# Kernel tuning notes

Hardware: AMD Instinct MI355X
Metric: run time of the kernel (lower is better)

The kernel has to match this reference:

```python
import jax, jax.numpy as jnp
import numpy as np

NUM_HEADS = 16
BLOCK_SIZE = 64


def setup_inputs() -> dict:
    key = jax.random.key(0)
    ks = jax.random.split(key, 5)
    B, S, C = 2, 2047, 1024
    return {
        "x": jax.random.normal(ks[0], (B, S, C), dtype=jnp.float32),
        "global_token": jax.random.normal(ks[1], (1, 1, C), dtype=jnp.float32),
        "qkv_w": jax.random.normal(ks[2], (3 * C, C), dtype=jnp.float32) * 0.02,
        "proj_w": jax.random.normal(ks[3], (C, C), dtype=jnp.float32) * 0.02,
        "proj_b": jax.random.normal(ks[4], (C,), dtype=jnp.float32) * 0.02,
    }


def reference(x, global_token, qkv_w, proj_w, proj_b):
    B, S, C = x.shape
    H = NUM_HEADS
    D = C // H
    scale = D ** -0.5
    # prepend global token -> N = S + 1
    g = jnp.broadcast_to(global_token, (B, 1, C))
    xg = jnp.concatenate([g, x], axis=1)
    N = S + 1
    # fused qkv projection (torch Linear: x @ W^T)
    qkv = (xg @ qkv_w.T).reshape(B, N, 3, H, D)
    qkv = jnp.transpose(qkv, (2, 0, 3, 1, 4))  # [3, B, H, N, D]
    q, k, v = qkv[0], qkv[1], qkv[2]
    # block-causal mask: query t sees key j iff block(j) <= block(t)
    blk = jnp.arange(N) // BLOCK_SIZE
    mask = blk[:, None] >= blk[None, :]  # [N, N]
    attn = jnp.einsum("bhqd,bhkd->bhqk", q, k) * scale
    attn = jnp.where(mask[None, None], attn, -jnp.inf)
    attn = jax.nn.softmax(attn, axis=-1)
    out = jnp.einsum("bhqk,bhkd->bhqd", attn, v)
    out = jnp.transpose(out, (0, 2, 1, 3)).reshape(B, N, C)
    out = out[:, 1:, :]  # drop global token
    return out @ proj_w.T + proj_b
```

## Files before the change

kernel.cpp:

```cpp
#include <hip/hip_runtime.h>
#include <math.h>

typedef _Float16 h16;
typedef _Float16 half8 __attribute__((ext_vector_type(8)));
typedef float f32x4 __attribute__((ext_vector_type(4)));

#define NB 2
#define NS 2047
#define NC 1024
#define NN 2048
#define NH 16
#define ND 64

__device__ __forceinline__ void gl_lds16(const h16* g, h16* l) {
  __builtin_amdgcn_global_load_lds((const __attribute__((address_space(1))) void*)g,
                                   (__attribute__((address_space(3))) void*)l, 16, 0, 0);
}
__device__ __forceinline__ f32x4 mfma16(half8 a, half8 b, f32x4 c) {
  return __builtin_amdgcn_mfma_f32_16x16x32_f16(a, b, c, 0, 0, 0);
}

__global__ __launch_bounds__(256) void cast_xg_k(
    const float* __restrict__ x, const float* __restrict__ g, h16* __restrict__ out) {
  size_t i = ((size_t)blockIdx.x * 256 + threadIdx.x) * 16;
  const int c = (int)(i & (NC - 1));
  const int n = (int)((i >> 10) & (NN - 1));
  const int b = (int)(i >> 21);
  const float* src = (n == 0) ? (g + c) : (x + ((size_t)b * NS + (n - 1)) * NC + c);
  h16 tmp[16];
#pragma unroll
  for (int j = 0; j < 4; ++j) {
    float4 f = ((const float4*)src)[j];
    tmp[4 * j + 0] = (h16)f.x; tmp[4 * j + 1] = (h16)f.y;
    tmp[4 * j + 2] = (h16)f.z; tmp[4 * j + 3] = (h16)f.w;
  }
  *(half8*)(out + i) = *(half8*)&tmp[0];
  *(half8*)(out + i + 8) = *(half8*)&tmp[8];
}

__global__ __launch_bounds__(256) void cast_f16_k(
    const float* __restrict__ in, h16* __restrict__ out) {
  size_t i = ((size_t)blockIdx.x * 256 + threadIdx.x) * 8;
  float4 f0 = ((const float4*)(in + i))[0];
  float4 f1 = ((const float4*)(in + i))[1];
  h16 tmp[8];
  tmp[0] = (h16)f0.x; tmp[1] = (h16)f0.y; tmp[2] = (h16)f0.z; tmp[3] = (h16)f0.w;
  tmp[4] = (h16)f1.x; tmp[5] = (h16)f1.y; tmp[6] = (h16)f1.z; tmp[7] = (h16)f1.w;
  *(half8*)(out + i) = *(half8*)&tmp[0];
}

__global__ __launch_bounds__(256) void gemm_qkv_h(
    const h16* __restrict__ A, const h16* __restrict__ W, h16* __restrict__ out) {
  __shared__ h16 As[128 * 32];
  __shared__ h16 Bs[128 * 32];
  const int tid = threadIdx.x;
  const int m0 = blockIdx.y * 128, j0 = blockIdx.x * 128;
  const int wid = tid >> 6, lane = tid & 63, l15 = lane & 15, quad = lane >> 4;
  const h16* ag = A + (size_t)(m0 + wid * 32 + (lane >> 2)) * NC + (lane & 3) * 8;
  const h16* bg = W + (size_t)(j0 + wid * 32 + (lane >> 2)) * NC + (lane & 3) * 8;
  h16* lA = &As[wid * 32 * 32];
  h16* lB = &Bs[wid * 32 * 32];
  f32x4 acc[2][8];
#pragma unroll
  for (int rt = 0; rt < 2; ++rt)
#pragma unroll
    for (int ct = 0; ct < 8; ++ct) acc[rt][ct] = (f32x4){0.f, 0.f, 0.f, 0.f};

  for (int k0 = 0; k0 < NC; k0 += 32) {
    __syncthreads();
    gl_lds16(ag + k0, lA);
    gl_lds16(ag + k0 + 16 * NC, lA + 16 * 32);
    gl_lds16(bg + k0, lB);
    gl_lds16(bg + k0 + 16 * NC, lB + 16 * 32);
    __syncthreads();
    half8 af0 = *(const half8*)&As[(wid * 32 + l15) * 32 + quad * 8];
    half8 af1 = *(const half8*)&As[(wid * 32 + 16 + l15) * 32 + quad * 8];
#pragma unroll
    for (int ct = 0; ct < 8; ++ct) {
      half8 bf = *(const half8*)&Bs[(ct * 16 + l15) * 32 + quad * 8];
      acc[0][ct] = mfma16(af0, bf, acc[0][ct]);
      acc[1][ct] = mfma16(af1, bf, acc[1][ct]);
    }
  }
#pragma unroll
  for (int rt = 0; rt < 2; ++rt)
#pragma unroll
    for (int ct = 0; ct < 8; ++ct)
#pragma unroll
      for (int r = 0; r < 4; ++r) {
        const int mm = m0 + wid * 32 + rt * 16 + quad * 4 + r;
        const int jj = j0 + ct * 16 + l15;
        out[(size_t)mm * (3 * NC) + jj] = (h16)acc[rt][ct][r];
      }
}

__global__ __launch_bounds__(256) void vtrans_k(
    const h16* __restrict__ qkvh, h16* __restrict__ vT) {
  __shared__ h16 ts[64 * 72];
  const int kb = blockIdx.x, h = blockIdx.y, b = blockIdx.z;
  const int t = threadIdx.x;
  const int key = t >> 2, co = (t & 3) * 16;
  const h16* src = qkvh + (size_t)(b * NN + kb * 64 + key) * (3 * NC) + 2 * NC + h * ND + co;
  half8 v0 = *(const half8*)src;
  half8 v1 = *(const half8*)(src + 8);
  *(half8*)&ts[key * 72 + co] = v0;
  *(half8*)&ts[key * 72 + co + 8] = v1;
  __syncthreads();
  const int d = t >> 2, ko = (t & 3) * 16;
  h16 buf[16];
#pragma unroll
  for (int i = 0; i < 16; ++i) buf[i] = ts[(ko + i) * 72 + d];
  h16* dst = vT + ((size_t)(b * NH + h) * ND + d) * NN + kb * 64 + ko;
  *(half8*)dst = *(half8*)&buf[0];
  *(half8*)(dst + 8) = *(half8*)&buf[8];
}

__device__ __forceinline__ void attn_tile(
    half8 aq0, half8 aq1, const h16* Ks, const h16* Vs, h16* Pw,
    int l15, int quad, f32x4* o, float* den) {
  f32x4 s[4];
#pragma unroll
  for (int ct = 0; ct < 4; ++ct) {
    half8 bk0 = *(const half8*)&Ks[(ct * 16 + l15) * 72 + quad * 8];
    half8 bk1 = *(const half8*)&Ks[(ct * 16 + l15) * 72 + 32 + quad * 8];
    f32x4 z = (f32x4){0.f, 0.f, 0.f, 0.f};
    z = mfma16(aq0, bk0, z);
    s[ct] = mfma16(aq1, bk1, z);
  }
#pragma unroll
  for (int ct = 0; ct < 4; ++ct)
#pragma unroll
    for (int r = 0; r < 4; ++r) {
      float p = __expf(s[ct][r] * 0.125f);
      den[r] += p;
      Pw[(quad * 4 + r) * 72 + ct * 16 + l15] = (h16)p;
    }
  half8 ap0 = *(const half8*)&Pw[l15 * 72 + quad * 8];
  half8 ap1 = *(const half8*)&Pw[l15 * 72 + 32 + quad * 8];
#pragma unroll
  for (int ct = 0; ct < 4; ++ct) {
    half8 bv0 = *(const half8*)&Vs[(ct * 16 + l15) * 72 + quad * 8];
    half8 bv1 = *(const half8*)&Vs[(ct * 16 + l15) * 72 + 32 + quad * 8];
    o[ct] = mfma16(ap0, bv0, o[ct]);
    o[ct] = mfma16(ap1, bv1, o[ct]);
  }
}

__global__ __launch_bounds__(256) void attn_h(
    const h16* __restrict__ qkvh, const h16* __restrict__ vT, h16* __restrict__ outp) {
  __shared__ h16 Ks[64 * 72];
  __shared__ h16 Vs[64 * 72];
  __shared__ h16 Ps[128 * 72];
  const int q1 = blockIdx.x;
  const int q2 = 31 - q1;
  const int h = blockIdx.y, b = blockIdx.z;
  const int tid = threadIdx.x, wid = tid >> 6, lane = tid & 63;
  const int l15 = lane & 15, quad = lane >> 4;
  const h16* q1src = qkvh + (size_t)(b * NN + q1 * 64 + wid * 16 + l15) * (3 * NC) + h * ND + quad * 8;
  const h16* q2src = qkvh + (size_t)(b * NN + q2 * 64 + wid * 16 + l15) * (3 * NC) + h * ND + quad * 8;
  half8 a1q0 = *(const half8*)q1src;
  half8 a1q1 = *(const half8*)(q1src + 32);
  half8 a2q0 = *(const half8*)q2src;
  half8 a2q1 = *(const half8*)(q2src + 32);
  f32x4 o1[4], o2[4];
  float d1[4] = {0.f, 0.f, 0.f, 0.f}, d2[4] = {0.f, 0.f, 0.f, 0.f};
#pragma unroll
  for (int ct = 0; ct < 4; ++ct) {
    o1[ct] = (f32x4){0.f, 0.f, 0.f, 0.f};
    o2[ct] = (f32x4){0.f, 0.f, 0.f, 0.f};
  }
  const int skey = tid >> 2, sco = (tid & 3) * 16;
  const h16* kbase = qkvh + (size_t)(b * NN + skey) * (3 * NC) + NC + h * ND + sco;
  const h16* vbase = vT + ((size_t)(b * NH + h) * ND + skey) * NN + sco;
  h16* P1 = &Ps[(wid * 16) * 72];
  h16* P2 = &Ps[(64 + wid * 16) * 72];

  for (int kb = 0; kb <= q2; ++kb) {
    const h16* kp = kbase + (size_t)kb * 64 * (3 * NC);
    half8 k0 = *(const half8*)kp;
    half8 k1 = *(const half8*)(kp + 8);
    const h16* vp = vbase + kb * 64;
    half8 v0 = *(const half8*)vp;
    half8 v1 = *(const half8*)(vp + 8);
    __syncthreads();
    *(half8*)&Ks[skey * 72 + sco] = k0; *(half8*)&Ks[skey * 72 + sco + 8] = k1;
    *(half8*)&Vs[skey * 72 + sco] = v0; *(half8*)&Vs[skey * 72 + sco + 8] = v1;
    __syncthreads();
    attn_tile(a2q0, a2q1, Ks, Vs, P2, l15, quad, o2, d2);
    if (kb <= q1) attn_tile(a1q0, a1q1, Ks, Vs, P1, l15, quad, o1, d1);
  }
#pragma unroll
  for (int r = 0; r < 4; ++r)
#pragma unroll
    for (int off = 1; off < 16; off <<= 1) {
      d1[r] += __shfl_xor(d1[r], off);
      d2[r] += __shfl_xor(d2[r], off);
    }
#pragma unroll
  for (int ct = 0; ct < 4; ++ct)
#pragma unroll
    for (int r = 0; r < 4; ++r) {
      const int n1 = q1 * 64 + wid * 16 + quad * 4 + r;
      const int n2 = q2 * 64 + wid * 16 + quad * 4 + r;
      outp[(size_t)(b * NN + n1) * NC + h * ND + ct * 16 + l15] = (h16)(o1[ct][r] / d1[r]);
      outp[(size_t)(b * NN + n2) * NC + h * ND + ct * 16 + l15] = (h16)(o2[ct][r] / d2[r]);
    }
}

__global__ __launch_bounds__(256) void gemm_proj_h(
    const h16* __restrict__ Ah, const h16* __restrict__ W,
    const float* __restrict__ bias, float* __restrict__ out) {
  __shared__ h16 As[64 * 32];
  __shared__ h16 Bs[128 * 32];
  const int tid = threadIdx.x;
  const int m0 = blockIdx.y * 64, j0 = blockIdx.x * 128;
  const int wid = tid >> 6, lane = tid & 63, l15 = lane & 15, quad = lane >> 4;
  int m = m0 + wid * 16 + (lane >> 2);
  if (m > NB * NS - 1) m = NB * NS - 1;
  const int bb = (m >= NS) ? 1 : 0;
  const h16* ag = Ah + (size_t)(bb * NN + m - bb * NS + 1) * NC + (lane & 3) * 8;
  const h16* bg = W + (size_t)(j0 + wid * 32 + (lane >> 2)) * NC + (lane & 3) * 8;
  h16* lA = &As[wid * 16 * 32];
  h16* lB = &Bs[wid * 32 * 32];
  f32x4 acc[8];
#pragma unroll
  for (int ct = 0; ct < 8; ++ct) acc[ct] = (f32x4){0.f, 0.f, 0.f, 0.f};

  for (int k0 = 0; k0 < NC; k0 += 32) {
    __syncthreads();
    gl_lds16(ag + k0, lA);
    gl_lds16(bg + k0, lB);
    gl_lds16(bg + k0 + 16 * NC, lB + 16 * 32);
    __syncthreads();
    half8 af = *(const half8*)&As[(wid * 16 + l15) * 32 + quad * 8];
#pragma unroll
    for (int ct = 0; ct < 8; ++ct) {
      half8 bf = *(const half8*)&Bs[(ct * 16 + l15) * 32 + quad * 8];
      acc[ct] = mfma16(af, bf, acc[ct]);
    }
  }
#pragma unroll
  for (int ct = 0; ct < 8; ++ct) {
    const float bv = bias[j0 + ct * 16 + l15];
#pragma unroll
    for (int r = 0; r < 4; ++r) {
      const int mm = m0 + wid * 16 + quad * 4 + r;
      if (mm < NB * NS)
        out[(size_t)mm * NC + j0 + ct * 16 + l15] = acc[ct][r] + bv;
    }
  }
}

extern "C" void kernel_launch(void* const* d_in, const int* in_sizes, int n_in,
                              void* d_out, int out_size, void* d_ws, size_t ws_size,
                              hipStream_t stream) {
  const float* x = (const float*)d_in[0];
  const float* g = (const float*)d_in[1];
  const float* qkv_w = (const float*)d_in[2];
  const float* proj_w = (const float*)d_in[3];
  const float* proj_b = (const float*)d_in[4];
  float* out = (float*)d_out;

  h16* xgh  = (h16*)d_ws;
  h16* w3h  = xgh + (size_t)NB * NN * NC;
  h16* wph  = w3h + (size_t)3 * NC * NC;
  h16* qkvh = wph + (size_t)NC * NC;
  h16* vTh  = qkvh + (size_t)NB * NN * 3 * NC;
  h16* attnh = vTh + (size_t)NB * NH * ND * NN;

  cast_xg_k<<<dim3(1024), 256, 0, stream>>>(x, g, xgh);
  cast_f16_k<<<dim3(1536), 256, 0, stream>>>(qkv_w, w3h);
  cast_f16_k<<<dim3(512), 256, 0, stream>>>(proj_w, wph);
  gemm_qkv_h<<<dim3(24, 32), 256, 0, stream>>>(xgh, w3h, qkvh);
  vtrans_k<<<dim3(32, NH, NB), 256, 0, stream>>>(qkvh, vTh);
  attn_h<<<dim3(16, NH, NB), 256, 0, stream>>>(qkvh, vTh, attnh);
  gemm_proj_h<<<dim3(8, 64), 256, 0, stream>>>(attnh, wph, proj_b, out);
}
```

Measured before the change: 204.0 us.

## Split attention KV loop across two blocks with merge kernel, prefetch K/V, fuse weight casts

The attention kernel now splits each query-pair's key-block loop between two blocks by even/odd key block. Each block writes unnormalized partial outputs and row denominators, and a new merge kernel sums and normalizes them. This doubles the attention grid to fill more CUs (512 blocks instead of 256), and the next K/V tile is prefetched into registers while the current tile is computed. A shared P buffer and a launch-bounds occupancy hint shrink LDS use. The two weight-cast launches are also fused into one, at the cost of an extra merge pass and more intermediate memory traffic.

```diff
diff --git a/kernel.cpp b/kernel.cpp
--- a/kernel.cpp
+++ b/kernel.cpp
@@ -38,11 +38,12 @@
   *(half8*)(out + i + 8) = *(half8*)&tmp[8];
 }
 
-__global__ __launch_bounds__(256) void cast_f16_k(
-    const float* __restrict__ in, h16* __restrict__ out) {
+__global__ __launch_bounds__(256) void cast_w_k(
+    const float* __restrict__ qw, const float* __restrict__ pw, h16* __restrict__ out) {
   size_t i = ((size_t)blockIdx.x * 256 + threadIdx.x) * 8;
-  float4 f0 = ((const float4*)(in + i))[0];
-  float4 f1 = ((const float4*)(in + i))[1];
+  const float* src = (i < (size_t)3 * NC * NC) ? (qw + i) : (pw + (i - (size_t)3 * NC * NC));
+  float4 f0 = ((const float4*)src)[0];
+  float4 f1 = ((const float4*)src)[1];
   h16 tmp[8];
   tmp[0] = (h16)f0.x; tmp[1] = (h16)f0.y; tmp[2] = (h16)f0.z; tmp[3] = (h16)f0.w;
   tmp[4] = (h16)f1.x; tmp[5] = (h16)f1.y; tmp[6] = (h16)f1.z; tmp[7] = (h16)f1.w;
@@ -146,13 +147,15 @@
   }
 }
 
-__global__ __launch_bounds__(256) void attn_h(
-    const h16* __restrict__ qkvh, const h16* __restrict__ vT, h16* __restrict__ outp) {
+__global__ __launch_bounds__(256, 4) void attn_h(
+    const h16* __restrict__ qkvh, const h16* __restrict__ vT,
+    h16* __restrict__ Op0, h16* __restrict__ Op1, float* __restrict__ denp) {
   __shared__ h16 Ks[64 * 72];
   __shared__ h16 Vs[64 * 72];
-  __shared__ h16 Ps[128 * 72];
-  const int q1 = blockIdx.x;
-  const int q2 = 31 - q1;
+  __shared__ h16 Ps[64 * 72];
+  const int pr = blockIdx.x & 15;
+  const int c = blockIdx.x >> 4;
+  const int q1 = pr, q2 = 31 - pr;
   const int h = blockIdx.y, b = blockIdx.z;
   const int tid = threadIdx.x, wid = tid >> 6, lane = tid & 63;
   const int l15 = lane & 15, quad = lane >> 4;
@@ -172,22 +175,26 @@
   const int skey = tid >> 2, sco = (tid & 3) * 16;
   const h16* kbase = qkvh + (size_t)(b * NN + skey) * (3 * NC) + NC + h * ND + sco;
   const h16* vbase = vT + ((size_t)(b * NH + h) * ND + skey) * NN + sco;
-  h16* P1 = &Ps[(wid * 16) * 72];
-  h16* P2 = &Ps[(64 + wid * 16) * 72];
-
-  for (int kb = 0; kb <= q2; ++kb) {
-    const h16* kp = kbase + (size_t)kb * 64 * (3 * NC);
-    half8 k0 = *(const half8*)kp;
-    half8 k1 = *(const half8*)(kp + 8);
-    const h16* vp = vbase + kb * 64;
-    half8 v0 = *(const half8*)vp;
-    half8 v1 = *(const half8*)(vp + 8);
+  h16* Pw = &Ps[(wid * 16) * 72];
+
+  int kb = c;
+  const h16* kp = kbase + (size_t)kb * (64 * 3 * NC);
+  const h16* vp = vbase + kb * 64;
+  half8 k0 = *(const half8*)kp, k1 = *(const half8*)(kp + 8);
+  half8 v0 = *(const half8*)vp, v1 = *(const half8*)(vp + 8);
+
+  for (; kb <= q2; kb += 2) {
     __syncthreads();
     *(half8*)&Ks[skey * 72 + sco] = k0; *(half8*)&Ks[skey * 72 + sco + 8] = k1;
     *(half8*)&Vs[skey * 72 + sco] = v0; *(half8*)&Vs[skey * 72 + sco + 8] = v1;
     __syncthreads();
-    attn_tile(a2q0, a2q1, Ks, Vs, P2, l15, quad, o2, d2);
-    if (kb <= q1) attn_tile(a1q0, a1q1, Ks, Vs, P1, l15, quad, o1, d1);
+    const int nkb = (kb + 2 <= q2) ? (kb + 2) : kb;
+    kp = kbase + (size_t)nkb * (64 * 3 * NC);
+    vp = vbase + nkb * 64;
+    k0 = *(const half8*)kp; k1 = *(const half8*)(kp + 8);
+    v0 = *(const half8*)vp; v1 = *(const half8*)(vp + 8);
+    attn_tile(a2q0, a2q1, Ks, Vs, Pw, l15, quad, o2, d2);
+    if (kb <= q1) attn_tile(a1q0, a1q1, Ks, Vs, Pw, l15, quad, o1, d1);
   }
 #pragma unroll
   for (int r = 0; r < 4; ++r)
@@ -196,15 +203,40 @@
       d1[r] += __shfl_xor(d1[r], off);
       d2[r] += __shfl_xor(d2[r], off);
     }
+  h16* op = (c == 0) ? Op0 : Op1;
+  const size_t rbase = (size_t)(b * NH + h) * NN;
+  float* dch = denp + (size_t)c * (NB * NH * NN);
 #pragma unroll
   for (int ct = 0; ct < 4; ++ct)
 #pragma unroll
     for (int r = 0; r < 4; ++r) {
       const int n1 = q1 * 64 + wid * 16 + quad * 4 + r;
       const int n2 = q2 * 64 + wid * 16 + quad * 4 + r;
-      outp[(size_t)(b * NN + n1) * NC + h * ND + ct * 16 + l15] = (h16)(o1[ct][r] / d1[r]);
-      outp[(size_t)(b * NN + n2) * NC + h * ND + ct * 16 + l15] = (h16)(o2[ct][r] / d2[r]);
-    }
+      op[(rbase + n1) * ND + ct * 16 + l15] = (h16)o1[ct][r];
+      op[(rbase + n2) * ND + ct * 16 + l15] = (h16)o2[ct][r];
+      if (ct == 0 && l15 == 0) {
+        dch[rbase + n1] = d1[r];
+        dch[rbase + n2] = d2[r];
+      }
+    }
+}
+
+__global__ __launch_bounds__(256) void merge_k(
+    const h16* __restrict__ Op0, const h16* __restrict__ Op1,
+    const float* __restrict__ denp, h16* __restrict__ attnh) {
+  const size_t t = (size_t)blockIdx.x * 256 + threadIdx.x;
+  const int d = (int)(t & 7) * 8;
+  const size_t row = t >> 3;
+  half8 a = *(const half8*)(Op0 + row * ND + d);
+  half8 bb8 = *(const half8*)(Op1 + row * ND + d);
+  const float inv = 1.f / (denp[row] + denp[(size_t)NB * NH * NN + row]);
+  h16 o[8];
+#pragma unroll
+  for (int j = 0; j < 8; ++j) o[j] = (h16)(((float)a[j] + (float)bb8[j]) * inv);
+  const int n = (int)(row & (NN - 1));
+  const int h = (int)((row >> 11) & (NH - 1));
+  const int b = (int)(row >> 15);
+  *(half8*)(attnh + (size_t)(b * NN + n) * NC + h * ND + d) = *(half8*)&o[0];
 }
 
 __global__ __launch_bounds__(256) void gemm_proj_h(
@@ -267,12 +299,15 @@
   h16* qkvh = wph + (size_t)NC * NC;
   h16* vTh  = qkvh + (size_t)NB * NN * 3 * NC;
   h16* attnh = vTh + (size_t)NB * NH * ND * NN;
+  h16* op1  = attnh + (size_t)NB * NN * NC;
+  float* den = (float*)(op1 + (size_t)NB * NN * NC);
+  h16* op0 = xgh;
 
   cast_xg_k<<<dim3(1024), 256, 0, stream>>>(x, g, xgh);
-  cast_f16_k<<<dim3(1536), 256, 0, stream>>>(qkv_w, w3h);
-  cast_f16_k<<<dim3(512), 256, 0, stream>>>(proj_w, wph);
+  cast_w_k<<<dim3(2048), 256, 0, stream>>>(qkv_w, proj_w, w3h);
   gemm_qkv_h<<<dim3(24, 32), 256, 0, stream>>>(xgh, w3h, qkvh);
   vtrans_k<<<dim3(32, NH, NB), 256, 0, stream>>>(qkvh, vTh);
-  attn_h<<<dim3(16, NH, NB), 256, 0, stream>>>(qkvh, vTh, attnh);
+  attn_h<<<dim3(32, NH, NB), 256, 0, stream>>>(qkvh, vTh, op0, op1, den);
+  merge_k<<<dim3(2048), 256, 0, stream>>>(op0, op1, den, attnh);
   gemm_proj_h<<<dim3(8, 64), 256, 0, stream>>>(attnh, wph, proj_b, out);
 }
```

After: 251.9 us. 23.5% more time.

## Double-buffer attention K/V via direct LDS loads and keep P in registers

Applied to the files above, without the earlier changes.

Rewrites the attention kernel to prefetch the next K/V tile with global_load_lds into a swizzled double buffer, so loads overlap compute and each iteration needs one barrier instead of two. It computes S transposed (K as the A operand) and redistributes the packed fp16 probabilities through lane shuffles rather than an LDS round-trip, and folds the softmax scale into Q. The output is staged through LDS so each row is written with 16-byte stores. It also merges the two weight cast kernels into one launch and flattens the attention grid with a launch bound of 2 blocks per SM.

```diff
diff --git a/kernel.cpp b/kernel.cpp
--- a/kernel.cpp
+++ b/kernel.cpp
@@ -3,6 +3,7 @@
 
 typedef _Float16 h16;
 typedef _Float16 half8 __attribute__((ext_vector_type(8)));
+typedef _Float16 half2t __attribute__((ext_vector_type(2)));
 typedef float f32x4 __attribute__((ext_vector_type(4)));
 
 #define NB 2
@@ -38,11 +39,12 @@
   *(half8*)(out + i + 8) = *(half8*)&tmp[8];
 }
 
-__global__ __launch_bounds__(256) void cast_f16_k(
-    const float* __restrict__ in, h16* __restrict__ out) {
+__global__ __launch_bounds__(256) void cast_w_k(
+    const float* __restrict__ qw, const float* __restrict__ pw, h16* __restrict__ out) {
   size_t i = ((size_t)blockIdx.x * 256 + threadIdx.x) * 8;
-  float4 f0 = ((const float4*)(in + i))[0];
-  float4 f1 = ((const float4*)(in + i))[1];
+  const float* src = (i < (size_t)3 * NC * NC) ? (qw + i) : (pw + (i - (size_t)3 * NC * NC));
+  float4 f0 = ((const float4*)src)[0];
+  float4 f1 = ((const float4*)src)[1];
   h16 tmp[8];
   tmp[0] = (h16)f0.x; tmp[1] = (h16)f0.y; tmp[2] = (h16)f0.z; tmp[3] = (h16)f0.w;
   tmp[4] = (h16)f1.x; tmp[5] = (h16)f1.y; tmp[6] = (h16)f1.z; tmp[7] = (h16)f1.w;
@@ -115,96 +117,139 @@
   *(half8*)(dst + 8) = *(half8*)&buf[8];
 }
 
-__device__ __forceinline__ void attn_tile(
-    half8 aq0, half8 aq1, const h16* Ks, const h16* Vs, h16* Pw,
-    int l15, int quad, f32x4* o, float* den) {
-  f32x4 s[4];
+__global__ __launch_bounds__(256, 2) void attn_h(
+    const h16* __restrict__ qkvh, const h16* __restrict__ vT, h16* __restrict__ outp) {
+  __shared__ h16 KV[4][64 * 64];
+  const int wg = blockIdx.x;
+  const int pr = wg >> 5;
+  const int bh = wg & 31;
+  const int b = bh >> 4, h = bh & 15;
+  const int q1 = pr, q2 = 31 - pr;
+  const int tid = threadIdx.x, w = tid >> 6, lane = tid & 63;
+  const int l15 = lane & 15, quad = lane >> 4;
+
+  const int srow = w * 8 + (lane >> 3);
+  const int schunk = (lane & 7) ^ (srow & 7);
+  const h16* kq = qkvh + ((size_t)(b * NN + srow) * 3 + 1) * NC + h * ND + schunk * 8;
+  const h16* vq = vT + ((size_t)(b * NH + h) * ND + srow) * NN + schunk * 8;
+  const int ldso = w * 512;
+
+  const h16* q1src = qkvh + (size_t)(b * NN + q1 * 64 + w * 16 + l15) * (3 * NC) + h * ND + quad * 8;
+  const h16* q2src = qkvh + (size_t)(b * NN + q2 * 64 + w * 16 + l15) * (3 * NC) + h * ND + quad * 8;
+  half8 b1lo = *(const half8*)q1src, b1hi = *(const half8*)(q1src + 32);
+  half8 b2lo = *(const half8*)q2src, b2hi = *(const half8*)(q2src + 32);
+  b1lo *= (h16)0.125f; b1hi *= (h16)0.125f;
+  b2lo *= (h16)0.125f; b2hi *= (h16)0.125f;
+
+  int aoff[4][2];
 #pragma unroll
   for (int ct = 0; ct < 4; ++ct) {
-    half8 bk0 = *(const half8*)&Ks[(ct * 16 + l15) * 72 + quad * 8];
-    half8 bk1 = *(const half8*)&Ks[(ct * 16 + l15) * 72 + 32 + quad * 8];
-    f32x4 z = (f32x4){0.f, 0.f, 0.f, 0.f};
-    z = mfma16(aq0, bk0, z);
-    s[ct] = mfma16(aq1, bk1, z);
-  }
-#pragma unroll
-  for (int ct = 0; ct < 4; ++ct)
-#pragma unroll
-    for (int r = 0; r < 4; ++r) {
-      float p = __expf(s[ct][r] * 0.125f);
-      den[r] += p;
-      Pw[(quad * 4 + r) * 72 + ct * 16 + l15] = (h16)p;
-    }
-  half8 ap0 = *(const half8*)&Pw[l15 * 72 + quad * 8];
-  half8 ap1 = *(const half8*)&Pw[l15 * 72 + 32 + quad * 8];
-#pragma unroll
-  for (int ct = 0; ct < 4; ++ct) {
-    half8 bv0 = *(const half8*)&Vs[(ct * 16 + l15) * 72 + quad * 8];
-    half8 bv1 = *(const half8*)&Vs[(ct * 16 + l15) * 72 + 32 + quad * 8];
-    o[ct] = mfma16(ap0, bv0, o[ct]);
-    o[ct] = mfma16(ap1, bv1, o[ct]);
-  }
-}
-
-__global__ __launch_bounds__(256) void attn_h(
-    const h16* __restrict__ qkvh, const h16* __restrict__ vT, h16* __restrict__ outp) {
-  __shared__ h16 Ks[64 * 72];
-  __shared__ h16 Vs[64 * 72];
-  __shared__ h16 Ps[128 * 72];
-  const int q1 = blockIdx.x;
-  const int q2 = 31 - q1;
-  const int h = blockIdx.y, b = blockIdx.z;
-  const int tid = threadIdx.x, wid = tid >> 6, lane = tid & 63;
-  const int l15 = lane & 15, quad = lane >> 4;
-  const h16* q1src = qkvh + (size_t)(b * NN + q1 * 64 + wid * 16 + l15) * (3 * NC) + h * ND + quad * 8;
-  const h16* q2src = qkvh + (size_t)(b * NN + q2 * 64 + wid * 16 + l15) * (3 * NC) + h * ND + quad * 8;
-  half8 a1q0 = *(const half8*)q1src;
-  half8 a1q1 = *(const half8*)(q1src + 32);
-  half8 a2q0 = *(const half8*)q2src;
-  half8 a2q1 = *(const half8*)(q2src + 32);
+    const int r = ct * 16 + l15;
+    aoff[ct][0] = r * 64 + ((quad ^ (l15 & 7)) * 8);
+    aoff[ct][1] = r * 64 + (((quad + 4) ^ (l15 & 7)) * 8);
+  }
+  const int L0 = ((quad & 1) << 5) + l15;
+  const int L1 = L0 + 16;
+  const bool cs = ((quad >> 1) & 1) != 0;
+
   f32x4 o1[4], o2[4];
-  float d1[4] = {0.f, 0.f, 0.f, 0.f}, d2[4] = {0.f, 0.f, 0.f, 0.f};
+  float den1 = 0.f, den2 = 0.f;
 #pragma unroll
   for (int ct = 0; ct < 4; ++ct) {
     o1[ct] = (f32x4){0.f, 0.f, 0.f, 0.f};
     o2[ct] = (f32x4){0.f, 0.f, 0.f, 0.f};
   }
-  const int skey = tid >> 2, sco = (tid & 3) * 16;
-  const h16* kbase = qkvh + (size_t)(b * NN + skey) * (3 * NC) + NC + h * ND + sco;
-  const h16* vbase = vT + ((size_t)(b * NH + h) * ND + skey) * NN + sco;
-  h16* P1 = &Ps[(wid * 16) * 72];
-  h16* P2 = &Ps[(64 + wid * 16) * 72];
-
+
+  h16 *Kc = &KV[0][0], *Vc = &KV[1][0], *Kn = &KV[2][0], *Vn = &KV[3][0];
+
+#define STAGE(Kd, Vd, kb)                                              \
+  {                                                                    \
+    const h16* kp_ = kq + (size_t)(kb) * (64 * 3 * NC);                \
+    const h16* vp_ = vq + (kb)*64;                                     \
+    gl_lds16(kp_, (Kd) + ldso);                                        \
+    gl_lds16(kp_ + (size_t)32 * 3 * NC, (Kd) + 2048 + ldso);           \
+    gl_lds16(vp_, (Vd) + ldso);                                        \
+    gl_lds16(vp_ + 32 * NN, (Vd) + 2048 + ldso);                       \
+  }
+
+#define TILE(bqlo, bqhi, o, den)                                        \
+  {                                                                     \
+    f32x4 s_[4];                                                        \
+    _Pragma("unroll") for (int ct = 0; ct < 4; ++ct) {                  \
+      f32x4 z_ = (f32x4){0.f, 0.f, 0.f, 0.f};                           \
+      z_ = mfma16(kA[ct][0], bqlo, z_);                                 \
+      s_[ct] = mfma16(kA[ct][1], bqhi, z_);                             \
+    }                                                                   \
+    int pk_[4][2];                                                      \
+    _Pragma("unroll") for (int ct = 0; ct < 4; ++ct) {                  \
+      float e0 = __expf(s_[ct][0]), e1 = __expf(s_[ct][1]);             \
+      float e2 = __expf(s_[ct][2]), e3 = __expf(s_[ct][3]);             \
+      den += (e0 + e1) + (e2 + e3);                                     \
+      pk_[ct][0] = __builtin_bit_cast(int, __builtin_amdgcn_cvt_pkrtz(e0, e1)); \
+      pk_[ct][1] = __builtin_bit_cast(int, __builtin_amdgcn_cvt_pkrtz(e2, e3)); \
+    }                                                                   \
+    int a0 = __shfl(pk_[0][0], L0), a1 = __shfl(pk_[0][1], L0);         \
+    int a2 = __shfl(pk_[0][0], L1), a3 = __shfl(pk_[0][1], L1);         \
+    int c0 = __shfl(pk_[1][0], L0), c1 = __shfl(pk_[1][1], L0);         \
+    int c2 = __shfl(pk_[1][0], L1), c3 = __shfl(pk_[1][1], L1);         \
+    int4 f0i = make_int4(cs ? c0 : a0, cs ? c1 : a1, cs ? c2 : a2, cs ? c3 : a3); \
+    a0 = __shfl(pk_[2][0], L0); a1 = __shfl(pk_[2][1], L0);             \
+    a2 = __shfl(pk_[2][0], L1); a3 = __shfl(pk_[2][1], L1);             \
+    c0 = __shfl(pk_[3][0], L0); c1 = __shfl(pk_[3][1], L0);             \
+    c2 = __shfl(pk_[3][0], L1); c3 = __shfl(pk_[3][1], L1);             \
+    int4 f1i = make_int4(cs ? c0 : a0, cs ? c1 : a1, cs ? c2 : a2, cs ? c3 : a3); \
+    half8 pf0 = __builtin_bit_cast(half8, f0i);                         \
+    half8 pf1 = __builtin_bit_cast(half8, f1i);                         \
+    _Pragma("unroll") for (int ct = 0; ct < 4; ++ct) {                  \
+      o[ct] = mfma16(vA[ct][0], pf0, o[ct]);                           \
+      o[ct] = mfma16(vA[ct][1], pf1, o[ct]);                           \
+    }                                                                   \
+  }
+
+  STAGE(Kc, Vc, 0);
   for (int kb = 0; kb <= q2; ++kb) {
-    const h16* kp = kbase + (size_t)kb * 64 * (3 * NC);
-    half8 k0 = *(const half8*)kp;
-    half8 k1 = *(const half8*)(kp + 8);
-    const h16* vp = vbase + kb * 64;
-    half8 v0 = *(const half8*)vp;
-    half8 v1 = *(const half8*)(vp + 8);
-    __syncthreads();
-    *(half8*)&Ks[skey * 72 + sco] = k0; *(half8*)&Ks[skey * 72 + sco + 8] = k1;
-    *(half8*)&Vs[skey * 72 + sco] = v0; *(half8*)&Vs[skey * 72 + sco + 8] = v1;
-    __syncthreads();
-    attn_tile(a2q0, a2q1, Ks, Vs, P2, l15, quad, o2, d2);
-    if (kb <= q1) attn_tile(a1q0, a1q1, Ks, Vs, P1, l15, quad, o1, d1);
-  }
-#pragma unroll
-  for (int r = 0; r < 4; ++r)
-#pragma unroll
-    for (int off = 1; off < 16; off <<= 1) {
-      d1[r] += __shfl_xor(d1[r], off);
-      d2[r] += __shfl_xor(d2[r], off);
+    __syncthreads();
+    if (kb < q2) STAGE(Kn, Vn, kb + 1);
+    half8 kA[4][2], vA[4][2];
+#pragma unroll
+    for (int ct = 0; ct < 4; ++ct) {
+      kA[ct][0] = *(const half8*)&Kc[aoff[ct][0]];
+      kA[ct][1] = *(const half8*)&Kc[aoff[ct][1]];
+      vA[ct][0] = *(const half8*)&Vc[aoff[ct][0]];
+      vA[ct][1] = *(const half8*)&Vc[aoff[ct][1]];
     }
-#pragma unroll
-  for (int ct = 0; ct < 4; ++ct)
-#pragma unroll
-    for (int r = 0; r < 4; ++r) {
-      const int n1 = q1 * 64 + wid * 16 + quad * 4 + r;
-      const int n2 = q2 * 64 + wid * 16 + quad * 4 + r;
-      outp[(size_t)(b * NN + n1) * NC + h * ND + ct * 16 + l15] = (h16)(o1[ct][r] / d1[r]);
-      outp[(size_t)(b * NN + n2) * NC + h * ND + ct * 16 + l15] = (h16)(o2[ct][r] / d2[r]);
-    }
+    TILE(b2lo, b2hi, o2, den2);
+    if (kb <= q1) TILE(b1lo, b1hi, o1, den1);
+    h16* t;
+    t = Kc; Kc = Kn; Kn = t;
+    t = Vc; Vc = Vn; Vn = t;
+  }
+
+  den1 += __shfl_xor(den1, 16); den1 += __shfl_xor(den1, 32);
+  den2 += __shfl_xor(den2, 16); den2 += __shfl_xor(den2, 32);
+  const float i1 = 1.f / den1, i2 = 1.f / den2;
+
+  __syncthreads();
+  h16* Es = &KV[0][0];
+  const int e2o = w * 1152, e1o = 4608 + w * 1152;
+#pragma unroll
+  for (int ct = 0; ct < 4; ++ct) {
+    int2 w2, w1;
+    w2.x = __builtin_bit_cast(int, __builtin_amdgcn_cvt_pkrtz(o2[ct][0] * i2, o2[ct][1] * i2));
+    w2.y = __builtin_bit_cast(int, __builtin_amdgcn_cvt_pkrtz(o2[ct][2] * i2, o2[ct][3] * i2));
+    w1.x = __builtin_bit_cast(int, __builtin_amdgcn_cvt_pkrtz(o1[ct][0] * i1, o1[ct][1] * i1));
+    w1.y = __builtin_bit_cast(int, __builtin_amdgcn_cvt_pkrtz(o1[ct][2] * i1, o1[ct][3] * i1));
+    *(int2*)&Es[e2o + l15 * 72 + ct * 16 + quad * 4] = w2;
+    *(int2*)&Es[e1o + l15 * 72 + ct * 16 + quad * 4] = w1;
+  }
+  half8 r20 = *(const half8*)&Es[e2o + l15 * 72 + quad * 8];
+  half8 r21 = *(const half8*)&Es[e2o + l15 * 72 + 32 + quad * 8];
+  half8 r10 = *(const half8*)&Es[e1o + l15 * 72 + quad * 8];
+  half8 r11 = *(const half8*)&Es[e1o + l15 * 72 + 32 + quad * 8];
+  h16* d2 = outp + (size_t)(b * NN + q2 * 64 + w * 16 + l15) * NC + h * ND + quad * 8;
+  h16* d1 = outp + (size_t)(b * NN + q1 * 64 + w * 16 + l15) * NC + h * ND + quad * 8;
+  *(half8*)d2 = r20; *(half8*)(d2 + 32) = r21;
+  *(half8*)d1 = r10; *(half8*)(d1 + 32) = r11;
 }
 
 __global__ __launch_bounds__(256) void gemm_proj_h(
@@ -269,10 +314,9 @@
   h16* attnh = vTh + (size_t)NB * NH * ND * NN;
 
   cast_xg_k<<<dim3(1024), 256, 0, stream>>>(x, g, xgh);
-  cast_f16_k<<<dim3(1536), 256, 0, stream>>>(qkv_w, w3h);
-  cast_f16_k<<<dim3(512), 256, 0, stream>>>(proj_w, wph);
+  cast_w_k<<<dim3(2048), 256, 0, stream>>>(qkv_w, proj_w, w3h);
   gemm_qkv_h<<<dim3(24, 32), 256, 0, stream>>>(xgh, w3h, qkvh);
   vtrans_k<<<dim3(32, NH, NB), 256, 0, stream>>>(qkvh, vTh);
-  attn_h<<<dim3(16, NH, NB), 256, 0, stream>>>(qkvh, vTh, attnh);
+  attn_h<<<dim3(512), 256, 0, stream>>>(qkvh, vTh, attnh);
   gemm_proj_h<<<dim3(8, 64), 256, 0, stream>>>(attnh, wph, proj_b, out);
 }
```

After: 185.7 us. -9.0%, faster.
